# Kernel tuning notes

Measured on AMD Instinct MI355X. Metric: run time of the kernel, lower is better.

The kernel has to match this reference:

```python
import jax, jax.numpy as jnp
import numpy as np

B, V, K, CL1_F = 8192, 1000, 5, 5
HID, OUT, NLAYERS = 256, 10, 4
BN_EPS = 1e-5


def _make_laplacian(rng):
    A = (rng.random((V, V)) < 0.01).astype(np.float32)
    A = np.triu(A, 1)
    A = A + A.T
    d = np.maximum(A.sum(1), 1.0)
    dinv = 1.0 / np.sqrt(d)
    Lap = np.eye(V, dtype=np.float32) - (dinv[:, None] * A * dinv[None, :])
    lmax = float(np.linalg.eigvalsh(Lap.astype(np.float64))[-1])
    return Lap.astype(np.float32), np.array([lmax], dtype=np.float32)


def setup_inputs() -> dict:
    key = jax.random.key(0)
    ks = jax.random.split(key, 16)
    rng = np.random.default_rng(0)
    Lap, lmax = _make_laplacian(rng)
    s = lambda fan_in: 1.0 / np.sqrt(fan_in)
    inp = {
        "x": jax.random.normal(ks[0], (B, V), dtype=jnp.float32),
        "L": jnp.asarray(Lap),
        "lmax": jnp.asarray(lmax),
        "cl1_W": jax.random.uniform(ks[1], (CL1_F, K), jnp.float32, -s(K), s(K)),
        "cl1_b": jax.random.uniform(ks[2], (CL1_F,), jnp.float32, -s(K), s(K)),
        "fc1_W": jax.random.uniform(ks[3], (HID, 625), jnp.float32, -s(625), s(625)),
        "fc1_b": jax.random.uniform(ks[4], (HID,), jnp.float32, -s(625), s(625)),
        "bn_gamma": jnp.ones((NLAYERS, HID), jnp.float32),
        "bn_beta": jnp.zeros((NLAYERS, HID), jnp.float32),
        "bn_mean": 0.1 * jax.random.normal(ks[5], (NLAYERS, HID), dtype=jnp.float32),
        "bn_var": jnp.ones((NLAYERS, HID), jnp.float32) + 0.1 * jax.random.uniform(ks[6], (NLAYERS, HID), dtype=jnp.float32),
        "lin1_W": jax.random.uniform(ks[7], (HID, HID), jnp.float32, -s(HID), s(HID)),
        "lin1_b": jax.random.uniform(ks[8], (HID,), jnp.float32, -s(HID), s(HID)),
        "lin2_W": jax.random.uniform(ks[9], (OUT, HID), jnp.float32, -s(HID), s(HID)),
        "lin2_b": jax.random.uniform(ks[10], (OUT,), jnp.float32, -s(HID), s(HID)),
    }
    return inp


def reference(x, L, lmax, cl1_W, cl1_b, fc1_W, fc1_b,
              bn_gamma, bn_beta, bn_mean, bn_var,
              lin1_W, lin1_b, lin2_W, lin2_b):
    # ---- graph_conv_cheby (Fin = 1) ----
    Lr = 2.0 * L / lmax[0] - jnp.eye(V, dtype=L.dtype)  # rescale_L
    x0 = x.T                              # [V, B]  (Fin*B with Fin=1)
    x1 = Lr @ x0
    basis = [x0, x1]
    for _ in range(2, K):                 # Chebyshev recursion T_k = 2 L T_{k-1} - T_{k-2}
        basis.append(2.0 * (Lr @ basis[-1]) - basis[-2])
    xk = jnp.stack(basis, 0)              # [K, V, B]
    feat = xk.transpose(2, 1, 0).reshape(B * V, K)       # [B*V, Fin*K]
    h = feat @ cl1_W.T + cl1_b            # cl1: Linear(5,5)
    h = jax.nn.relu(h.reshape(B, V, CL1_F))
    # ---- graph_max_pool p=8 over node dim ----
    h = h.reshape(B, V // 8, 8, CL1_F).max(axis=2)       # [B, 125, 5]
    h = h.reshape(B, 625)
    h = h @ fc1_W.T + fc1_b               # [B, 256]
    # ---- per-layer BN (eval) + ReLU (dropout inactive in eval); convs never applied ----
    xs = []
    for i in range(NLAYERS):
        h = (h - bn_mean[i]) * (bn_gamma[i] / jnp.sqrt(bn_var[i] + BN_EPS)) + bn_beta[i]
        h = jax.nn.relu(h)
        xs.append(h)
    # ---- JumpingKnowledge (max) ----
    z = jnp.max(jnp.stack(xs, 0), axis=0)
    z = jax.nn.relu(z @ lin1_W.T + lin1_b)
    out = z @ lin2_W.T + lin2_b
    return jax.nn.log_softmax(out, axis=-1)
```

## Files before the change

kernel.cpp:

```cpp
#include <hip/hip_runtime.h>

typedef unsigned int u32;
typedef unsigned short u16;
typedef unsigned long long u64;

typedef __attribute__((ext_vector_type(8))) short s8v;
typedef __attribute__((ext_vector_type(4))) float f4v;

#define B_SZ   8192
#define V_SZ   1000
#define KCH    5
#define MAXDEG 32

__device__ __forceinline__ u16 f2bf(float f) {
    u32 u = __float_as_uint(f);
    u32 r = (u + 0x7FFFu + ((u >> 16) & 1u)) >> 16;
    return (u16)r;
}
__device__ __forceinline__ float bf2f(u16 h) { return __uint_as_float(((u32)h) << 16); }

__global__ __launch_bounds__(256) void k_prep(const float* __restrict__ L,
                                              const float* __restrict__ lmax,
                                              u32* __restrict__ packed,
                                              int* __restrict__ cnts,
                                              float* __restrict__ diagw,
                                              const float* __restrict__ fc1W,
                                              const float* __restrict__ lin1W,
                                              const float* __restrict__ gam,
                                              const float* __restrict__ bet,
                                              const float* __restrict__ mea,
                                              const float* __restrict__ var,
                                              u16* __restrict__ fc1w_b,
                                              u16* __restrict__ lin1w_b,
                                              float* __restrict__ bn_a,
                                              float* __restrict__ bn_c) {
    if (blockIdx.x < 250) {
        int wid  = threadIdx.x >> 6;
        int lane = threadIdx.x & 63;
        int row  = blockIdx.x * 4 + wid;
        if (row >= V_SZ) return;
        float s = 2.0f / lmax[0];
        const float* Lrow = L + (u64)row * V_SZ;
        int cnt = 0;
        for (int c0 = 0; c0 < V_SZ; c0 += 64) {
            int c = c0 + lane;
            float val = 0.0f;
            if (c < V_SZ && c != row) val = Lrow[c];
            bool nz = (val != 0.0f);
            u64 m = __ballot(nz);
            int pos = cnt + __popcll(m & ((1ull << lane) - 1ull));
            if (nz && pos < MAXDEG) {
                u32 w = __float_as_uint(val * s);
                packed[((pos >> 2) * V_SZ + row) * 4 + (pos & 3)] = (w & 0xFFFFFC00u) | (u32)c;
            }
            cnt += __popcll(m);
        }
        int cc = cnt < MAXDEG ? cnt : MAXDEG;
        for (int e = cc + lane; e < MAXDEG; e += 64)
            packed[((e >> 2) * V_SZ + row) * 4 + (e & 3)] = 0;
        if (lane == 0) {
            cnts[row]  = cc;
            diagw[row] = s * Lrow[row] - 1.0f;
        }
    } else {
        int t = (blockIdx.x - 250) * 256 + threadIdx.x;
        if (t < 256 * 640) {
            int r = t / 640, c = t - r * 640;
            fc1w_b[t] = (c < 625) ? f2bf(fc1W[r * 625 + c]) : (u16)0;
        }
        if (t < 256 * 256) lin1w_b[t] = f2bf(lin1W[t]);
        if (t < 4 * 256) {
            float a = gam[t] * rsqrtf(var[t] + 1e-5f);
            bn_a[t] = a;
            bn_c[t] = bet[t] - mea[t] * a;
        }
    }
}

__global__ __launch_bounds__(512, 4) void k_cheby(const float* __restrict__ x,
                                                  const int4* __restrict__ packed4,
                                                  const int* __restrict__ cnts,
                                                  const float* __restrict__ diagw,
                                                  const float* __restrict__ cl1W,
                                                  const float* __restrict__ cl1b,
                                                  u16* __restrict__ pooled) {
    __shared__ float4 buf[2][V_SZ];
    __shared__ float cws[25];
    __shared__ float cbs[5];
    int t  = threadIdx.x;
    int b0 = blockIdx.x * 4;

    if (t < 25) cws[t] = cl1W[t];
    if (t < 5)  cbs[t] = cl1b[t];

    const int  v1   = t + 512;
    const bool val1 = (v1 < V_SZ);

    float d0 = diagw[t];
    int   n0 = (cnts[t] + 3) >> 2;
    float d1 = 0.f;
    int   n1 = 0;
    if (val1) { d1 = diagw[v1]; n1 = (cnts[v1] + 3) >> 2; }

    float4 pm1_0, pm2_0, pm1_1, pm2_1;
    {
        float4 a;
        a.x = x[(u64)(b0 + 0) * V_SZ + t];
        a.y = x[(u64)(b0 + 1) * V_SZ + t];
        a.z = x[(u64)(b0 + 2) * V_SZ + t];
        a.w = x[(u64)(b0 + 3) * V_SZ + t];
        buf[0][t] = a;
        pm1_0 = a; pm2_0 = a;
        float4 b = make_float4(0.f, 0.f, 0.f, 0.f);
        if (val1) {
            b.x = x[(u64)(b0 + 0) * V_SZ + v1];
            b.y = x[(u64)(b0 + 1) * V_SZ + v1];
            b.z = x[(u64)(b0 + 2) * V_SZ + v1];
            b.w = x[(u64)(b0 + 3) * V_SZ + v1];
            buf[0][v1] = b;
        }
        pm1_1 = b; pm2_1 = b;
    }
    __syncthreads();

    float4 feat0[5], feat1[5];
#pragma unroll
    for (int f = 0; f < 5; ++f) {
        float w = cws[f * 5];
        feat0[f] = make_float4(w * pm1_0.x, w * pm1_0.y, w * pm1_0.z, w * pm1_0.w);
        feat1[f] = make_float4(w * pm1_1.x, w * pm1_1.y, w * pm1_1.z, w * pm1_1.w);
    }

#pragma unroll
    for (int k = 1; k < KCH; ++k) {
        const float4* prevb = buf[(k - 1) & 1];
        float4*       curb  = buf[k & 1];

        {
            float4 a = make_float4(d0 * pm1_0.x, d0 * pm1_0.y,
                                   d0 * pm1_0.z, d0 * pm1_0.w);
            int4 pw = packed4[t];
            for (int q = 0; q < n0; ++q) {
                int4 pwn = pw;
                if (q + 1 < n0) pwn = packed4[(q + 1) * V_SZ + t];
                float4 g0 = prevb[(u32)pw.x & 1023u];
                float4 g1 = prevb[(u32)pw.y & 1023u];
                float4 g2 = prevb[(u32)pw.z & 1023u];
                float4 g3 = prevb[(u32)pw.w & 1023u];
                float w0 = __uint_as_float((u32)pw.x & 0xFFFFFC00u);
                float w1 = __uint_as_float((u32)pw.y & 0xFFFFFC00u);
                float w2 = __uint_as_float((u32)pw.z & 0xFFFFFC00u);
                float w3 = __uint_as_float((u32)pw.w & 0xFFFFFC00u);
                a.x = fmaf(w0, g0.x, a.x); a.y = fmaf(w0, g0.y, a.y);
                a.z = fmaf(w0, g0.z, a.z); a.w = fmaf(w0, g0.w, a.w);
                a.x = fmaf(w1, g1.x, a.x); a.y = fmaf(w1, g1.y, a.y);
                a.z = fmaf(w1, g1.z, a.z); a.w = fmaf(w1, g1.w, a.w);
                a.x = fmaf(w2, g2.x, a.x); a.y = fmaf(w2, g2.y, a.y);
                a.z = fmaf(w2, g2.z, a.z); a.w = fmaf(w2, g2.w, a.w);
                a.x = fmaf(w3, g3.x, a.x); a.y = fmaf(w3, g3.y, a.y);
                a.z = fmaf(w3, g3.z, a.z); a.w = fmaf(w3, g3.w, a.w);
                pw = pwn;
            }
            if (k >= 2) {
                a.x = fmaf(2.0f, a.x, -pm2_0.x);
                a.y = fmaf(2.0f, a.y, -pm2_0.y);
                a.z = fmaf(2.0f, a.z, -pm2_0.z);
                a.w = fmaf(2.0f, a.w, -pm2_0.w);
            }
            curb[t] = a;
            pm2_0 = pm1_0; pm1_0 = a;
#pragma unroll
            for (int f = 0; f < 5; ++f) {
                float w = cws[f * 5 + k];
                feat0[f].x = fmaf(w, a.x, feat0[f].x);
                feat0[f].y = fmaf(w, a.y, feat0[f].y);
                feat0[f].z = fmaf(w, a.z, feat0[f].z);
                feat0[f].w = fmaf(w, a.w, feat0[f].w);
            }
        }
        if (val1) {
            float4 a = make_float4(d1 * pm1_1.x, d1 * pm1_1.y,
                                   d1 * pm1_1.z, d1 * pm1_1.w);
            int4 pw = packed4[v1];
            for (int q = 0; q < n1; ++q) {
                int4 pwn = pw;
                if (q + 1 < n1) pwn = packed4[(q + 1) * V_SZ + v1];
                float4 g0 = prevb[(u32)pw.x & 1023u];
                float4 g1 = prevb[(u32)pw.y & 1023u];
                float4 g2 = prevb[(u32)pw.z & 1023u];
                float4 g3 = prevb[(u32)pw.w & 1023u];
                float w0 = __uint_as_float((u32)pw.x & 0xFFFFFC00u);
                float w1 = __uint_as_float((u32)pw.y & 0xFFFFFC00u);
                float w2 = __uint_as_float((u32)pw.z & 0xFFFFFC00u);
                float w3 = __uint_as_float((u32)pw.w & 0xFFFFFC00u);
                a.x = fmaf(w0, g0.x, a.x); a.y = fmaf(w0, g0.y, a.y);
                a.z = fmaf(w0, g0.z, a.z); a.w = fmaf(w0, g0.w, a.w);
                a.x = fmaf(w1, g1.x, a.x); a.y = fmaf(w1, g1.y, a.y);
                a.z = fmaf(w1, g1.z, a.z); a.w = fmaf(w1, g1.w, a.w);
                a.x = fmaf(w2, g2.x, a.x); a.y = fmaf(w2, g2.y, a.y);
                a.z = fmaf(w2, g2.z, a.z); a.w = fmaf(w2, g2.w, a.w);
                a.x = fmaf(w3, g3.x, a.x); a.y = fmaf(w3, g3.y, a.y);
                a.z = fmaf(w3, g3.z, a.z); a.w = fmaf(w3, g3.w, a.w);
                pw = pwn;
            }
            if (k >= 2) {
                a.x = fmaf(2.0f, a.x, -pm2_1.x);
                a.y = fmaf(2.0f, a.y, -pm2_1.y);
                a.z = fmaf(2.0f, a.z, -pm2_1.z);
                a.w = fmaf(2.0f, a.w, -pm2_1.w);
            }
            curb[v1] = a;
            pm2_1 = pm1_1; pm1_1 = a;
#pragma unroll
            for (int f = 0; f < 5; ++f) {
                float w = cws[f * 5 + k];
                feat1[f].x = fmaf(w, a.x, feat1[f].x);
                feat1[f].y = fmaf(w, a.y, feat1[f].y);
                feat1[f].z = fmaf(w, a.z, feat1[f].z);
                feat1[f].w = fmaf(w, a.w, feat1[f].w);
            }
        }
        __syncthreads();
    }

#pragma unroll
    for (int f = 0; f < 5; ++f) {
#pragma unroll
        for (int b = 0; b < 4; ++b) {
            float c0 = (b == 0) ? feat0[f].x : (b == 1) ? feat0[f].y
                     : (b == 2) ? feat0[f].z : feat0[f].w;
            float s0 = fmaxf(c0 + cbs[f], 0.0f);
            s0 = fmaxf(s0, __shfl_xor(s0, 1));
            s0 = fmaxf(s0, __shfl_xor(s0, 2));
            s0 = fmaxf(s0, __shfl_xor(s0, 4));
            if ((t & 7) == 0)
                pooled[(u64)(b0 + b) * 640 + (t >> 3) * 5 + f] = f2bf(s0);

            float c1 = (b == 0) ? feat1[f].x : (b == 1) ? feat1[f].y
                     : (b == 2) ? feat1[f].z : feat1[f].w;
            float s1 = val1 ? fmaxf(c1 + cbs[f], 0.0f) : 0.0f;
            s1 = fmaxf(s1, __shfl_xor(s1, 1));
            s1 = fmaxf(s1, __shfl_xor(s1, 2));
            s1 = fmaxf(s1, __shfl_xor(s1, 4));
            if ((t & 7) == 0 && val1)
                pooled[(u64)(b0 + b) * 640 + (v1 >> 3) * 5 + f] = f2bf(s1);
        }
    }
    if (t < 60) {
        int b = t / 15, c = 625 + (t % 15);
        pooled[(u64)(b0 + b) * 640 + c] = 0;
    }
}

__global__ __launch_bounds__(256) void k_tail(const u16* __restrict__ A,
                                              const u16* __restrict__ W0,
                                              const float* __restrict__ b0v,
                                              const float* __restrict__ bn_a,
                                              const float* __restrict__ bn_c,
                                              const u16* __restrict__ W1,
                                              const float* __restrict__ b1v,
                                              const float* __restrict__ W2,
                                              const float* __restrict__ b2v,
                                              float* __restrict__ out) {
    __shared__ u16   As[64][72];
    __shared__ u16   Bs[256][72];
    __shared__ u16   zs[64][264];
    __shared__ float w2s[2560];
    __shared__ float b2s[10];
    int t    = threadIdx.x;
    int lane = t & 63;
    int wid  = t >> 6;
    int r0   = blockIdx.x * 64;

    for (int c = t; c < 2560; c += 256) w2s[c] = W2[c];
    if (t < 10) b2s[t] = b2v[t];

    f4v acc[16];
#pragma unroll
    for (int j = 0; j < 16; ++j) acc[j] = (f4v){0.f, 0.f, 0.f, 0.f};

    for (int k0 = 0; k0 < 640; k0 += 64) {
        int4 ra[2], rb[8];
#pragma unroll
        for (int i = 0; i < 2; ++i) {
            int c = t + i * 256, row = c >> 3, kc = c & 7;
            ra[i] = *(const int4*)(A + (u64)(r0 + row) * 640 + k0 + kc * 8);
        }
#pragma unroll
        for (int i = 0; i < 8; ++i) {
            int c = t + i * 256, row = c >> 3, kc = c & 7;
            rb[i] = *(const int4*)(W0 + (u64)row * 640 + k0 + kc * 8);
        }
        __syncthreads();
#pragma unroll
        for (int i = 0; i < 2; ++i) {
            int c = t + i * 256, row = c >> 3, kc = c & 7;
            *(int4*)(&As[row][kc * 8]) = ra[i];
        }
#pragma unroll
        for (int i = 0; i < 8; ++i) {
            int c = t + i * 256, row = c >> 3, kc = c & 7;
            *(int4*)(&Bs[row][kc * 8]) = rb[i];
        }
        __syncthreads();
#pragma unroll
        for (int ks = 0; ks < 2; ++ks) {
            int kq = ks * 32 + (lane >> 4) * 8;
            s8v af = *(const s8v*)(&As[wid * 16 + (lane & 15)][kq]);
#pragma unroll
            for (int nt = 0; nt < 16; ++nt) {
                s8v bf = *(const s8v*)(&Bs[nt * 16 + (lane & 15)][kq]);
                acc[nt] = __builtin_amdgcn_mfma_f32_16x16x32_bf16(af, bf, acc[nt], 0, 0, 0);
            }
        }
    }
#pragma unroll
    for (int nt = 0; nt < 16; ++nt) {
        int col = nt * 16 + (lane & 15);
        float bv = b0v[col];
        float a_[4], c_[4];
#pragma unroll
        for (int i = 0; i < 4; ++i) {
            a_[i] = bn_a[i * 256 + col];
            c_[i] = bn_c[i * 256 + col];
        }
        int rb_ = wid * 16 + (lane >> 4) * 4;
#pragma unroll
        for (int r = 0; r < 4; ++r) {
            float h = acc[nt][r] + bv, z = 0.0f;
#pragma unroll
            for (int i = 0; i < 4; ++i) {
                h = fmaxf(fmaf(a_[i], h, c_[i]), 0.0f);
                z = fmaxf(z, h);
            }
            zs[rb_ + r][col] = f2bf(z);
        }
    }
    __syncthreads();

#pragma unroll
    for (int j = 0; j < 16; ++j) acc[j] = (f4v){0.f, 0.f, 0.f, 0.f};
    for (int k0 = 0; k0 < 256; k0 += 64) {
        int4 rb[8];
#pragma unroll
        for (int i = 0; i < 8; ++i) {
            int c = t + i * 256, row = c >> 3, kc = c & 7;
            rb[i] = *(const int4*)(W1 + (u64)row * 256 + k0 + kc * 8);
        }
        __syncthreads();
#pragma unroll
        for (int i = 0; i < 8; ++i) {
            int c = t + i * 256, row = c >> 3, kc = c & 7;
            *(int4*)(&Bs[row][kc * 8]) = rb[i];
        }
        __syncthreads();
#pragma unroll
        for (int ks = 0; ks < 2; ++ks) {
            int kqr = ks * 32 + (lane >> 4) * 8;
            s8v af = *(const s8v*)(&zs[wid * 16 + (lane & 15)][k0 + kqr]);
#pragma unroll
            for (int nt = 0; nt < 16; ++nt) {
                s8v bf = *(const s8v*)(&Bs[nt * 16 + (lane & 15)][kqr]);
                acc[nt] = __builtin_amdgcn_mfma_f32_16x16x32_bf16(af, bf, acc[nt], 0, 0, 0);
            }
        }
    }
#pragma unroll
    for (int nt = 0; nt < 16; ++nt) {
        int col = nt * 16 + (lane & 15);
        float bv = b1v[col];
        int rb_ = wid * 16 + (lane >> 4) * 4;
#pragma unroll
        for (int r = 0; r < 4; ++r)
            zs[rb_ + r][col] = f2bf(fmaxf(acc[nt][r] + bv, 0.0f));
    }
    __syncthreads();

    {
        int row = t >> 2, sub = t & 3;
        float a10[10];
#pragma unroll
        for (int o = 0; o < 10; ++o) a10[o] = 0.0f;
        const u32* zrow = (const u32*)(&zs[row][0]);
        for (int kk = sub * 32; kk < sub * 32 + 32; ++kk) {
            u32 pz = zrow[kk];
            float z0 = bf2f((u16)(pz & 0xFFFFu));
            float z1 = bf2f((u16)(pz >> 16));
#pragma unroll
            for (int o = 0; o < 10; ++o) {
                a10[o] = fmaf(z0, w2s[o * 256 + kk * 2], a10[o]);
                a10[o] = fmaf(z1, w2s[o * 256 + kk * 2 + 1], a10[o]);
            }
        }
#pragma unroll
        for (int o = 0; o < 10; ++o) {
            a10[o] += __shfl_xor(a10[o], 1);
            a10[o] += __shfl_xor(a10[o], 2);
        }
        if (sub == 0) {
            float l[10], mx = -1e30f;
#pragma unroll
            for (int o = 0; o < 10; ++o) { l[o] = a10[o] + b2s[o]; mx = fmaxf(mx, l[o]); }
            float s = 0.0f;
#pragma unroll
            for (int o = 0; o < 10; ++o) s += expf(l[o] - mx);
            float ls = logf(s);
            float* orow = out + (u64)(r0 + row) * 10;
#pragma unroll
            for (int o = 0; o < 10; ++o) orow[o] = l[o] - mx - ls;
        }
    }
}

extern "C" void kernel_launch(void* const* d_in, const int* in_sizes, int n_in,
                              void* d_out, int out_size, void* d_ws, size_t ws_size,
                              hipStream_t stream) {
    const float* x    = (const float*)d_in[0];
    const float* L    = (const float*)d_in[1];
    const float* lmax = (const float*)d_in[2];
    const float* cl1W = (const float*)d_in[3];
    const float* cl1b = (const float*)d_in[4];
    const float* fc1W = (const float*)d_in[5];
    const float* fc1b = (const float*)d_in[6];
    const float* gam  = (const float*)d_in[7];
    const float* bet  = (const float*)d_in[8];
    const float* mea  = (const float*)d_in[9];
    const float* var  = (const float*)d_in[10];
    const float* l1W  = (const float*)d_in[11];
    const float* l1b  = (const float*)d_in[12];
    const float* l2W  = (const float*)d_in[13];
    const float* l2b  = (const float*)d_in[14];

    char* ws = (char*)d_ws;
    u32*   packed  = (u32*)(ws + 0);
    int*   cnts    = (int*)(ws + 131072);
    float* diagw   = (float*)(ws + 135168);
    float* bn_a    = (float*)(ws + 139264);
    float* bn_c    = (float*)(ws + 143360);
    u16*   fc1w_b  = (u16*)(ws + 147456);
    u16*   lin1w_b = (u16*)(ws + 475136);
    u16*   pooled  = (u16*)(ws + 606208);
    float* outp    = (float*)d_out;

    k_prep<<<dim3(890), dim3(256), 0, stream>>>(L, lmax, packed, cnts, diagw,
                                                fc1W, l1W, gam, bet, mea, var,
                                                fc1w_b, lin1w_b, bn_a, bn_c);
    k_cheby<<<dim3(2048), dim3(512), 0, stream>>>(x, (const int4*)packed, cnts, diagw,
                                                  cl1W, cl1b, pooled);
    k_tail<<<dim3(128), dim3(256), 0, stream>>>(pooled, fc1w_b, fc1b, bn_a, bn_c,
                                                lin1w_b, l1b, l2W, l2b, outp);
}
```

Measured before the change: 239.0 us.

## Process eight batch columns per Chebyshev block with one thread per node

```diff
diff --git a/kernel.cpp b/kernel.cpp
--- a/kernel.cpp
+++ b/kernel.cpp
@@ -77,147 +77,97 @@
     }
 }
 
-__global__ __launch_bounds__(512, 4) void k_cheby(const float* __restrict__ x,
-                                                  const int4* __restrict__ packed4,
-                                                  const int* __restrict__ cnts,
-                                                  const float* __restrict__ diagw,
-                                                  const float* __restrict__ cl1W,
-                                                  const float* __restrict__ cl1b,
-                                                  u16* __restrict__ pooled) {
-    __shared__ float4 buf[2][V_SZ];
+__global__ __launch_bounds__(1024) void k_cheby(const float* __restrict__ x,
+                                                const int4* __restrict__ packed4,
+                                                const int* __restrict__ cnts,
+                                                const float* __restrict__ diagw,
+                                                const float* __restrict__ cl1W,
+                                                const float* __restrict__ cl1b,
+                                                u16* __restrict__ pooled) {
+    __shared__ float buf[2][V_SZ * 8];
     __shared__ float cws[25];
     __shared__ float cbs[5];
     int t  = threadIdx.x;
-    int b0 = blockIdx.x * 4;
+    int b0 = blockIdx.x * 8;
 
     if (t < 25) cws[t] = cl1W[t];
     if (t < 5)  cbs[t] = cl1b[t];
 
-    const int  v1   = t + 512;
-    const bool val1 = (v1 < V_SZ);
-
-    float d0 = diagw[t];
-    int   n0 = (cnts[t] + 3) >> 2;
-    float d1 = 0.f;
-    int   n1 = 0;
-    if (val1) { d1 = diagw[v1]; n1 = (cnts[v1] + 3) >> 2; }
-
-    float4 pm1_0, pm2_0, pm1_1, pm2_1;
-    {
-        float4 a;
-        a.x = x[(u64)(b0 + 0) * V_SZ + t];
-        a.y = x[(u64)(b0 + 1) * V_SZ + t];
-        a.z = x[(u64)(b0 + 2) * V_SZ + t];
-        a.w = x[(u64)(b0 + 3) * V_SZ + t];
-        buf[0][t] = a;
-        pm1_0 = a; pm2_0 = a;
-        float4 b = make_float4(0.f, 0.f, 0.f, 0.f);
-        if (val1) {
-            b.x = x[(u64)(b0 + 0) * V_SZ + v1];
-            b.y = x[(u64)(b0 + 1) * V_SZ + v1];
-            b.z = x[(u64)(b0 + 2) * V_SZ + v1];
-            b.w = x[(u64)(b0 + 3) * V_SZ + v1];
-            buf[0][v1] = b;
-        }
-        pm1_1 = b; pm2_1 = b;
-    }
+    const bool own = (t < V_SZ);
+
+    float d0 = 0.0f;
+    int   n0 = 0;
+    if (own) { d0 = diagw[t]; n0 = (cnts[t] + 3) >> 2; }
+
+    float4 pm1l, pm1h, pm2l, pm2h;
+    pm1l = make_float4(0.f, 0.f, 0.f, 0.f);
+    pm1h = pm1l;
+    if (own) {
+        pm1l.x = x[(u64)(b0 + 0) * V_SZ + t];
+        pm1l.y = x[(u64)(b0 + 1) * V_SZ + t];
+        pm1l.z = x[(u64)(b0 + 2) * V_SZ + t];
+        pm1l.w = x[(u64)(b0 + 3) * V_SZ + t];
+        pm1h.x = x[(u64)(b0 + 4) * V_SZ + t];
+        pm1h.y = x[(u64)(b0 + 5) * V_SZ + t];
+        pm1h.z = x[(u64)(b0 + 6) * V_SZ + t];
+        pm1h.w = x[(u64)(b0 + 7) * V_SZ + t];
+        *(float4*)(&buf[0][t * 8])     = pm1l;
+        *(float4*)(&buf[0][t * 8 + 4]) = pm1h;
+    }
+    pm2l = pm1l; pm2h = pm1h;
     __syncthreads();
 
-    float4 feat0[5], feat1[5];
+    float4 fl[5], fh[5];
 #pragma unroll
     for (int f = 0; f < 5; ++f) {
         float w = cws[f * 5];
-        feat0[f] = make_float4(w * pm1_0.x, w * pm1_0.y, w * pm1_0.z, w * pm1_0.w);
-        feat1[f] = make_float4(w * pm1_1.x, w * pm1_1.y, w * pm1_1.z, w * pm1_1.w);
+        fl[f] = make_float4(w * pm1l.x, w * pm1l.y, w * pm1l.z, w * pm1l.w);
+        fh[f] = make_float4(w * pm1h.x, w * pm1h.y, w * pm1h.z, w * pm1h.w);
     }
 
 #pragma unroll
     for (int k = 1; k < KCH; ++k) {
-        const float4* prevb = buf[(k - 1) & 1];
-        float4*       curb  = buf[k & 1];
-
-        {
-            float4 a = make_float4(d0 * pm1_0.x, d0 * pm1_0.y,
-                                   d0 * pm1_0.z, d0 * pm1_0.w);
+        const float* prevb = buf[(k - 1) & 1];
+        float*       curb  = buf[k & 1];
+
+        if (own) {
+            float4 al = make_float4(d0 * pm1l.x, d0 * pm1l.y, d0 * pm1l.z, d0 * pm1l.w);
+            float4 ah = make_float4(d0 * pm1h.x, d0 * pm1h.y, d0 * pm1h.z, d0 * pm1h.w);
             int4 pw = packed4[t];
             for (int q = 0; q < n0; ++q) {
                 int4 pwn = pw;
                 if (q + 1 < n0) pwn = packed4[(q + 1) * V_SZ + t];
-                float4 g0 = prevb[(u32)pw.x & 1023u];
-                float4 g1 = prevb[(u32)pw.y & 1023u];
-                float4 g2 = prevb[(u32)pw.z & 1023u];
-                float4 g3 = prevb[(u32)pw.w & 1023u];
-                float w0 = __uint_as_float((u32)pw.x & 0xFFFFFC00u);
-                float w1 = __uint_as_float((u32)pw.y & 0xFFFFFC00u);
-                float w2 = __uint_as_float((u32)pw.z & 0xFFFFFC00u);
-                float w3 = __uint_as_float((u32)pw.w & 0xFFFFFC00u);
-                a.x = fmaf(w0, g0.x, a.x); a.y = fmaf(w0, g0.y, a.y);
-                a.z = fmaf(w0, g0.z, a.z); a.w = fmaf(w0, g0.w, a.w);
-                a.x = fmaf(w1, g1.x, a.x); a.y = fmaf(w1, g1.y, a.y);
-                a.z = fmaf(w1, g1.z, a.z); a.w = fmaf(w1, g1.w, a.w);
-                a.x = fmaf(w2, g2.x, a.x); a.y = fmaf(w2, g2.y, a.y);
-                a.z = fmaf(w2, g2.z, a.z); a.w = fmaf(w2, g2.w, a.w);
-                a.x = fmaf(w3, g3.x, a.x); a.y = fmaf(w3, g3.y, a.y);
-                a.z = fmaf(w3, g3.z, a.z); a.w = fmaf(w3, g3.w, a.w);
+#pragma unroll
+                for (int e = 0; e < 4; ++e) {
+                    u32 ent = (u32)((e == 0) ? pw.x : (e == 1) ? pw.y : (e == 2) ? pw.z : pw.w);
+                    float w = __uint_as_float(ent & 0xFFFFFC00u);
+                    const float4* p = (const float4*)(prevb + (ent & 1023u) * 8);
+                    float4 gl = p[0];
+                    float4 gh = p[1];
+                    al.x = fmaf(w, gl.x, al.x); al.y = fmaf(w, gl.y, al.y);
+                    al.z = fmaf(w, gl.z, al.z); al.w = fmaf(w, gl.w, al.w);
+                    ah.x = fmaf(w, gh.x, ah.x); ah.y = fmaf(w, gh.y, ah.y);
+                    ah.z = fmaf(w, gh.z, ah.z); ah.w = fmaf(w, gh.w, ah.w);
+                }
                 pw = pwn;
             }
             if (k >= 2) {
-                a.x = fmaf(2.0f, a.x, -pm2_0.x);
-                a.y = fmaf(2.0f, a.y, -pm2_0.y);
-                a.z = fmaf(2.0f, a.z, -pm2_0.z);
-                a.w = fmaf(2.0f, a.w, -pm2_0.w);
-            }
-            curb[t] = a;
-            pm2_0 = pm1_0; pm1_0 = a;
+                al.x = fmaf(2.0f, al.x, -pm2l.x); al.y = fmaf(2.0f, al.y, -pm2l.y);
+                al.z = fmaf(2.0f, al.z, -pm2l.z); al.w = fmaf(2.0f, al.w, -pm2l.w);
+                ah.x = fmaf(2.0f, ah.x, -pm2h.x); ah.y = fmaf(2.0f, ah.y, -pm2h.y);
+                ah.z = fmaf(2.0f, ah.z, -pm2h.z); ah.w = fmaf(2.0f, ah.w, -pm2h.w);
+            }
+            *(float4*)(&curb[t * 8])     = al;
+            *(float4*)(&curb[t * 8 + 4]) = ah;
+            pm2l = pm1l; pm2h = pm1h;
+            pm1l = al;   pm1h = ah;
 #pragma unroll
             for (int f = 0; f < 5; ++f) {
                 float w = cws[f * 5 + k];
-                feat0[f].x = fmaf(w, a.x, feat0[f].x);
-                feat0[f].y = fmaf(w, a.y, feat0[f].y);
-                feat0[f].z = fmaf(w, a.z, feat0[f].z);
-                feat0[f].w = fmaf(w, a.w, feat0[f].w);
-            }
-        }
-        if (val1) {
-            float4 a = make_float4(d1 * pm1_1.x, d1 * pm1_1.y,
-                                   d1 * pm1_1.z, d1 * pm1_1.w);
-            int4 pw = packed4[v1];
-            for (int q = 0; q < n1; ++q) {
-                int4 pwn = pw;
-                if (q + 1 < n1) pwn = packed4[(q + 1) * V_SZ + v1];
-                float4 g0 = prevb[(u32)pw.x & 1023u];
-                float4 g1 = prevb[(u32)pw.y & 1023u];
-                float4 g2 = prevb[(u32)pw.z & 1023u];
-                float4 g3 = prevb[(u32)pw.w & 1023u];
-                float w0 = __uint_as_float((u32)pw.x & 0xFFFFFC00u);
-                float w1 = __uint_as_float((u32)pw.y & 0xFFFFFC00u);
-                float w2 = __uint_as_float((u32)pw.z & 0xFFFFFC00u);
-                float w3 = __uint_as_float((u32)pw.w & 0xFFFFFC00u);
-                a.x = fmaf(w0, g0.x, a.x); a.y = fmaf(w0, g0.y, a.y);
-                a.z = fmaf(w0, g0.z, a.z); a.w = fmaf(w0, g0.w, a.w);
-                a.x = fmaf(w1, g1.x, a.x); a.y = fmaf(w1, g1.y, a.y);
-                a.z = fmaf(w1, g1.z, a.z); a.w = fmaf(w1, g1.w, a.w);
-                a.x = fmaf(w2, g2.x, a.x); a.y = fmaf(w2, g2.y, a.y);
-                a.z = fmaf(w2, g2.z, a.z); a.w = fmaf(w2, g2.w, a.w);
-                a.x = fmaf(w3, g3.x, a.x); a.y = fmaf(w3, g3.y, a.y);
-                a.z = fmaf(w3, g3.z, a.z); a.w = fmaf(w3, g3.w, a.w);
-                pw = pwn;
-            }
-            if (k >= 2) {
-                a.x = fmaf(2.0f, a.x, -pm2_1.x);
-                a.y = fmaf(2.0f, a.y, -pm2_1.y);
-                a.z = fmaf(2.0f, a.z, -pm2_1.z);
-                a.w = fmaf(2.0f, a.w, -pm2_1.w);
-            }
-            curb[v1] = a;
-            pm2_1 = pm1_1; pm1_1 = a;
-#pragma unroll
-            for (int f = 0; f < 5; ++f) {
-                float w = cws[f * 5 + k];
-                feat1[f].x = fmaf(w, a.x, feat1[f].x);
-                feat1[f].y = fmaf(w, a.y, feat1[f].y);
-                feat1[f].z = fmaf(w, a.z, feat1[f].z);
-                feat1[f].w = fmaf(w, a.w, feat1[f].w);
+                fl[f].x = fmaf(w, al.x, fl[f].x); fl[f].y = fmaf(w, al.y, fl[f].y);
+                fl[f].z = fmaf(w, al.z, fl[f].z); fl[f].w = fmaf(w, al.w, fl[f].w);
+                fh[f].x = fmaf(w, ah.x, fh[f].x); fh[f].y = fmaf(w, ah.y, fh[f].y);
+                fh[f].z = fmaf(w, ah.z, fh[f].z); fh[f].w = fmaf(w, ah.w, fh[f].w);
             }
         }
         __syncthreads();
@@ -226,27 +176,20 @@
 #pragma unroll
     for (int f = 0; f < 5; ++f) {
 #pragma unroll
-        for (int b = 0; b < 4; ++b) {
-            float c0 = (b == 0) ? feat0[f].x : (b == 1) ? feat0[f].y
-                     : (b == 2) ? feat0[f].z : feat0[f].w;
-            float s0 = fmaxf(c0 + cbs[f], 0.0f);
-            s0 = fmaxf(s0, __shfl_xor(s0, 1));
-            s0 = fmaxf(s0, __shfl_xor(s0, 2));
-            s0 = fmaxf(s0, __shfl_xor(s0, 4));
-            if ((t & 7) == 0)
-                pooled[(u64)(b0 + b) * 640 + (t >> 3) * 5 + f] = f2bf(s0);
-
-            float c1 = (b == 0) ? feat1[f].x : (b == 1) ? feat1[f].y
-                     : (b == 2) ? feat1[f].z : feat1[f].w;
-            float s1 = val1 ? fmaxf(c1 + cbs[f], 0.0f) : 0.0f;
-            s1 = fmaxf(s1, __shfl_xor(s1, 1));
-            s1 = fmaxf(s1, __shfl_xor(s1, 2));
-            s1 = fmaxf(s1, __shfl_xor(s1, 4));
-            if ((t & 7) == 0 && val1)
-                pooled[(u64)(b0 + b) * 640 + (v1 >> 3) * 5 + f] = f2bf(s1);
-        }
-    }
-    if (t < 60) {
+        for (int b = 0; b < 8; ++b) {
+            float c0 = (b == 0) ? fl[f].x : (b == 1) ? fl[f].y
+                     : (b == 2) ? fl[f].z : (b == 3) ? fl[f].w
+                     : (b == 4) ? fh[f].x : (b == 5) ? fh[f].y
+                     : (b == 6) ? fh[f].z : fh[f].w;
+            float s = own ? fmaxf(c0 + cbs[f], 0.0f) : 0.0f;
+            s = fmaxf(s, __shfl_xor(s, 1));
+            s = fmaxf(s, __shfl_xor(s, 2));
+            s = fmaxf(s, __shfl_xor(s, 4));
+            if ((t & 7) == 0 && own)
+                pooled[(u64)(b0 + b) * 640 + (t >> 3) * 5 + f] = f2bf(s);
+        }
+    }
+    if (t < 120) {
         int b = t / 15, c = 625 + (t % 15);
         pooled[(u64)(b0 + b) * 640 + c] = 0;
     }
@@ -445,8 +388,8 @@
     k_prep<<<dim3(890), dim3(256), 0, stream>>>(L, lmax, packed, cnts, diagw,
                                                 fc1W, l1W, gam, bet, mea, var,
                                                 fc1w_b, lin1w_b, bn_a, bn_c);
-    k_cheby<<<dim3(2048), dim3(512), 0, stream>>>(x, (const int4*)packed, cnts, diagw,
-                                                  cl1W, cl1b, pooled);
+    k_cheby<<<dim3(1024), dim3(1024), 0, stream>>>(x, (const int4*)packed, cnts, diagw,
+                                                   cl1W, cl1b, pooled);
     k_tail<<<dim3(128), dim3(256), 0, stream>>>(pooled, fc1w_b, fc1b, bn_a, bn_c,
                                                 lin1w_b, l1b, l2W, l2b, outp);
 }
```

Result: slower. 256.4 us (+7.3%).
